# Kernel tuning notes

Measured on AMD Instinct MI355X. Metric: run time of the kernel, lower is better.

Reference implementation:

```python
import jax, jax.numpy as jnp
import numpy as np
from jax import lax

B, T, C = 4, 2048, 2048
HK, HV = 16, 16
DK, DV = 128, 128
KW = 4  # conv kernel width
KEY_DIM = HK * DK      # 2048
VAL_DIM = HV * DV      # 2048
QKV_DIM = 2 * KEY_DIM + VAL_DIM  # 6144
EPS_RMS = 1e-6
EPS_NORM = 1e-12


def setup_inputs() -> dict:
    key = jax.random.key(0)
    ks = jax.random.split(key, 7)
    s = 0.02
    x = jax.random.normal(ks[0], (B, T, C), dtype=jnp.float32)
    positions = jnp.broadcast_to(jnp.arange(T, dtype=jnp.int64 if jax.config.jax_enable_x64 else jnp.int32), (B, T))
    W_qkvz = jax.random.normal(ks[1], (C, QKV_DIM + VAL_DIM), dtype=jnp.float32) * s
    W_b = jax.random.normal(ks[2], (C, HV), dtype=jnp.float32) * s
    W_a = jax.random.normal(ks[3], (C, HV), dtype=jnp.float32) * s
    conv_w = jax.random.normal(ks[4], (QKV_DIM, 1, KW), dtype=jnp.float32) * 0.1
    norm_w = jnp.ones((DV,), dtype=jnp.float32)
    W_out = jax.random.normal(ks[5], (VAL_DIM, C), dtype=jnp.float32) * s
    return {"x": x, "positions": positions, "W_qkvz": W_qkvz, "W_b": W_b,
            "W_a": W_a, "conv_w": conv_w, "norm_w": norm_w, "W_out": W_out}


def _l2norm(u):
    n = jnp.sqrt(jnp.sum(u * u, axis=-1, keepdims=True))
    return u / jnp.maximum(n, EPS_NORM)


def _forward(x, W_qkvz, W_b, W_a, conv_w, norm_w, W_out):
    qkvz = x @ W_qkvz                               # [B,T,QKV+VAL]
    qkv, z = qkvz[..., :QKV_DIM], qkvz[..., QKV_DIM:]
    z = z.reshape(B, T, HV, DV)
    beta = jax.nn.sigmoid(x @ W_b)                  # [B,T,HV]
    alpha = jax.nn.sigmoid(x @ W_a)                 # [B,T,HV]

    # depthwise causal conv1d (padding K-1 then truncate to T)
    xc = jnp.transpose(qkv, (0, 2, 1))              # [B,QKV_DIM,T]
    xc = lax.conv_general_dilated(xc, conv_w, window_strides=(1,),
                                  padding=[(KW - 1, 0)],
                                  feature_group_count=QKV_DIM,
                                  dimension_numbers=("NCH", "OIH", "NCH"))
    qkv = jnp.transpose(jax.nn.silu(xc), (0, 2, 1))  # [B,T,QKV_DIM]

    q = _l2norm(qkv[..., :KEY_DIM].reshape(B, T, HK, DK))
    k = _l2norm(qkv[..., KEY_DIM:2 * KEY_DIM].reshape(B, T, HK, DK))
    v = qkv[..., 2 * KEY_DIM:].reshape(B, T, HV, DV)

    def step(state, inp):
        q_t, k_t, v_t, b_t, a_t = inp               # [B,H,DK],[B,H,DK],[B,H,DV],[B,H],[B,H]
        state = a_t[:, :, None, None] * state + \
                b_t[:, :, None, None] * (k_t[..., :, None] * v_t[:, :, None, :])
        out = jnp.einsum('bhk,bhkv->bhv', q_t, state)
        return state, out

    state0 = jnp.zeros((B, HK, DK, DV), dtype=x.dtype)
    seq = (jnp.moveaxis(q, 1, 0), jnp.moveaxis(k, 1, 0), jnp.moveaxis(v, 1, 0),
           jnp.moveaxis(beta, 1, 0), jnp.moveaxis(alpha, 1, 0))
    _, outs = lax.scan(step, state0, seq)           # [T,B,H,DV]
    out = jnp.moveaxis(outs, 0, 1)                  # [B,T,H,DV]

    # RMSNorm over head_v_dim (fp32), gated by sigmoid(z)
    of = out.astype(jnp.float32)
    rms = jnp.mean(of * of, axis=-1, keepdims=True)
    out = ((of * lax.rsqrt(rms + EPS_RMS)) * norm_w).astype(out.dtype)
    out = out * jax.nn.sigmoid(z)
    return out.reshape(B, T, VAL_DIM) @ W_out


def reference(x, positions, W_qkvz, W_b, W_a, conv_w, norm_w, W_out):
    return _forward(x, W_qkvz, W_b, W_a, conv_w, norm_w, W_out)
```

## Files before the change

kernel.cpp:

```cpp
#include <hip/hip_runtime.h>
#include <hip/hip_bf16.h>

typedef __bf16 bf16_t;
typedef __attribute__((ext_vector_type(8))) __bf16 bf16x8;
typedef __attribute__((ext_vector_type(4))) float floatx4;
typedef __attribute__((ext_vector_type(16))) float floatx16;


__device__ __forceinline__ void gload16(const void* g, void* l) {
  __builtin_amdgcn_global_load_lds(
      (const __attribute__((address_space(1))) void*)g,
      (__attribute__((address_space(3))) void*)l, 16, 0, 0);
}

__global__ __launch_bounds__(256) void k_cast_bf16(const float* __restrict__ in,
                                                   bf16_t* __restrict__ out) {
  long i = ((long)blockIdx.x * 256 + threadIdx.x) * 8;
  const float4 a = *(const float4*)(in + i);
  const float4 b = *(const float4*)(in + i + 4);
  bf16x8 o;
  o[0] = (bf16_t)a.x; o[1] = (bf16_t)a.y; o[2] = (bf16_t)a.z; o[3] = (bf16_t)a.w;
  o[4] = (bf16_t)b.x; o[5] = (bf16_t)b.y; o[6] = (bf16_t)b.z; o[7] = (bf16_t)b.w;
  *(bf16x8*)(out + i) = o;
}

__global__ void k_transpose_cast(const float* __restrict__ in, bf16_t* __restrict__ out,
                                 int R, int Ccols) {
  __shared__ float tile[32][33];
  int c0 = blockIdx.x * 32, r0 = blockIdx.y * 32;
  for (int i = threadIdx.y; i < 32; i += 8)
    tile[i][threadIdx.x] = in[(long)(r0 + i) * Ccols + c0 + threadIdx.x];
  __syncthreads();
  for (int i = threadIdx.y; i < 32; i += 8)
    out[(long)(c0 + i) * R + r0 + threadIdx.x] = (bf16_t)tile[threadIdx.x][i];
}

__global__ void k_transpose_f32(const float* __restrict__ in, float* __restrict__ out,
                                int R, int Ccols) {
  int r = blockIdx.x * blockDim.x + threadIdx.x;
  if (r < R)
    for (int c = 0; c < Ccols; ++c) out[(long)c * R + r] = in[(long)r * Ccols + c];
}

__global__ __launch_bounds__(256) void k_beta_alpha(const float* __restrict__ x,
                                                    const float* __restrict__ WbT,
                                                    const float* __restrict__ WaT,
                                                    float* __restrict__ beta,
                                                    float* __restrict__ alpha) {
  extern __shared__ float xs[];
  const long row0 = (long)blockIdx.x * 16;
  const int tid = threadIdx.x;
  {
    const float4* src = (const float4*)(x + row0 * 2048);
    float4* dst = (float4*)xs;
    for (int i = tid; i < 16 * 512; i += 256) dst[i] = src[i];
  }
  __syncthreads();
  const int wv = tid >> 6, lane = tid & 63;
  for (int oo = 0; oo < 8; ++oo) {
    const int o = wv * 8 + oo;
    const float* Wrow = (o < 16) ? (WbT + (long)o * 2048) : (WaT + (long)(o - 16) * 2048);
    float acc[16];
#pragma unroll
    for (int r = 0; r < 16; ++r) acc[r] = 0.f;
    for (int kc = 0; kc < 8; ++kc) {
      const float4 w4 = *(const float4*)(Wrow + kc * 256 + lane * 4);
#pragma unroll
      for (int r = 0; r < 16; ++r) {
        const float4 xv = *(const float4*)&xs[r * 2048 + kc * 256 + lane * 4];
        acc[r] += w4.x * xv.x + w4.y * xv.y + w4.z * xv.z + w4.w * xv.w;
      }
    }
#pragma unroll
    for (int r = 0; r < 16; ++r) {
      float s = acc[r];
      for (int off = 32; off; off >>= 1) s += __shfl_down(s, off);
      if (lane == 0) {
        const long row = row0 + r;
        const int b = (int)(row >> 11), t = (int)(row & 2047);
        const float sig = 1.f / (1.f + __expf(-s));
        float* dst = (o < 16) ? beta : alpha;
        dst[((long)(b * 16 + (o & 15))) * 2048 + t] = sig;
      }
    }
  }
}

template <typename OUT_T>
__global__ __launch_bounds__(512, 2) void k_gemm256(const bf16_t* __restrict__ A,
                                                    const bf16_t* __restrict__ Bt,
                                                    OUT_T* __restrict__ C,
                                                    int N, int K, int lda) {
  extern __shared__ char gsm[];
  const int m0 = blockIdx.y * 256, n0 = blockIdx.x * 256;
  const int tid = threadIdx.x;
  const int w = tid >> 6, l = tid & 63;
  const int wm = w >> 2, wn = w & 3;
  const int l31 = l & 31, l5 = l >> 5;

  const bf16_t* asrc[4];
  const bf16_t* bsrc[4];
  int dofs[4];
#pragma unroll
  for (int t = 0; t < 4; ++t) {
    int c = t * 512 + tid;
    int row = c >> 3, cs = (c & 7) ^ (row & 7);
    asrc[t] = A + (long)(m0 + row) * lda + cs * 8;
    bsrc[t] = Bt + (long)(n0 + row) * K + cs * 8;
    dofs[t] = c * 16;
  }

  auto STAGE = [&](int buf, int k0) {
    char* ab = gsm + buf * 65536;
    char* bb = ab + 32768;
#pragma unroll
    for (int t = 0; t < 4; ++t) {
      gload16(asrc[t] + k0, ab + dofs[t]);
      gload16(bsrc[t] + k0, bb + dofs[t]);
    }
  };

  floatx16 acc[4][2] = {};
  STAGE(0, 0);
  const int NK = K >> 6;
  for (int kt = 0; kt < NK; ++kt) {
    __syncthreads();
    if (kt + 1 < NK) STAGE((kt + 1) & 1, (kt + 1) << 6);
    const char* As_ = gsm + (kt & 1) * 65536;
    const char* Bs_ = As_ + 32768;
#pragma unroll
    for (int ks = 0; ks < 4; ++ks) {
      bf16x8 af[4], bfr[2];
#pragma unroll
      for (int mi = 0; mi < 4; ++mi) {
        const int r = wm * 128 + mi * 32 + l31;
        af[mi] = *(const bf16x8*)(As_ + r * 128 + (((ks * 2 + l5) ^ (r & 7)) << 4));
      }
#pragma unroll
      for (int ni = 0; ni < 2; ++ni) {
        const int r = wn * 64 + ni * 32 + l31;
        bfr[ni] = *(const bf16x8*)(Bs_ + r * 128 + (((ks * 2 + l5) ^ (r & 7)) << 4));
      }
      __builtin_amdgcn_s_setprio(1);
#pragma unroll
      for (int mi = 0; mi < 4; ++mi)
#pragma unroll
        for (int ni = 0; ni < 2; ++ni)
          acc[mi][ni] = __builtin_amdgcn_mfma_f32_32x32x16_bf16(af[mi], bfr[ni], acc[mi][ni], 0, 0, 0);
      __builtin_amdgcn_s_setprio(0);
    }
  }
  const int crow0 = m0 + wm * 128 + 4 * l5;
  const int ccol = n0 + wn * 64 + l31;
#pragma unroll
  for (int mi = 0; mi < 4; ++mi)
#pragma unroll
    for (int ni = 0; ni < 2; ++ni)
#pragma unroll
      for (int reg = 0; reg < 16; ++reg) {
        const int row = crow0 + mi * 32 + (reg & 3) + 8 * (reg >> 2);
        C[(long)row * N + ccol + ni * 32] = (OUT_T)acc[mi][ni][reg];
      }
}

__global__ __launch_bounds__(256) void k_conv(const bf16_t* __restrict__ qkvz,
                                              const float* __restrict__ conv_w,
                                              bf16_t* __restrict__ q, bf16_t* __restrict__ k,
                                              bf16_t* __restrict__ v) {
  int row = blockIdx.x;
  int b = row >> 11, t = row & 2047;
  __shared__ float ys[6144];
  __shared__ float gsum[32][9];
  __shared__ float norms[32];
  const int c0 = threadIdx.x * 8;
  for (int c8 = c0; c8 < 6144; c8 += 2048) {
    bf16x8 xr[4];
#pragma unroll
    for (int w2 = 0; w2 < 4; ++w2) {
      int tt = t - 3 + w2;
      bf16x8 zr = {};
      xr[w2] = (tt >= 0) ? *(const bf16x8*)&qkvz[((long)(b * 2048 + tt)) * 8192 + c8] : zr;
    }
#pragma unroll
    for (int j = 0; j < 8; ++j) {
      float4 wv = *(const float4*)&conv_w[(c8 + j) * 4];
      float a = (float)xr[0][j] * wv.x + (float)xr[1][j] * wv.y +
                (float)xr[2][j] * wv.z + (float)xr[3][j] * wv.w;
      ys[c8 + j] = a / (1.f + __expf(-a));
    }
  }
  __syncthreads();
  {
    int g = threadIdx.x >> 3, j = threadIdx.x & 7;
    float s = 0.f;
#pragma unroll
    for (int e = 0; e < 16; ++e) {
      float yv = ys[g * 128 + j * 16 + e];
      s += yv * yv;
    }
    gsum[g][j] = s;
  }
  __syncthreads();
  if (threadIdx.x < 32) {
    float s = 0.f;
#pragma unroll
    for (int j = 0; j < 8; j++) s += gsum[threadIdx.x][j];
    norms[threadIdx.x] = 1.f / fmaxf(sqrtf(s), 1e-12f);
  }
  __syncthreads();
  for (int c8 = c0; c8 < 6144; c8 += 2048) {
    float scale;
    bf16_t* dst;
    if (c8 < 2048) {
      int h = c8 >> 7;
      scale = norms[h];
      dst = q + (((long)(b * 16 + h)) * 2048 + t) * 128 + (c8 & 127);
    } else if (c8 < 4096) {
      int h = (c8 - 2048) >> 7;
      scale = norms[16 + h];
      dst = k + (((long)(b * 16 + h)) * 2048 + t) * 128 + (c8 & 127);
    } else {
      scale = 1.f;
      int h = (c8 - 4096) >> 7;
      dst = v + (((long)(b * 16 + h)) * 2048 + t) * 128 + (c8 & 127);
    }
    bf16x8 o;
#pragma unroll
    for (int j = 0; j < 8; ++j) o[j] = (bf16_t)(ys[c8 + j] * scale);
    *(bf16x8*)dst = o;
  }
}

__global__ __launch_bounds__(256) void k_tr_kv(const bf16_t* __restrict__ kv,
                                               const bf16_t* __restrict__ vv,
                                               bf16_t* __restrict__ qkvz) {
  __shared__ bf16_t t_lds[64 * 136];
  int bh = blockIdx.x >> 5, tc = blockIdx.x & 31;
  int t0 = tc * 64;
  int tid = threadIdx.x;
#pragma unroll
  for (int pass = 0; pass < 2; ++pass) {
    const bf16_t* src = (pass == 0 ? kv : vv) + (long)bh * 2048 * 128 + (long)t0 * 128;
    int r = tid >> 2, sc = (tid & 3) * 32;
    bf16x8 x0 = *(const bf16x8*)(src + (long)r * 128 + sc);
    bf16x8 x1 = *(const bf16x8*)(src + (long)r * 128 + sc + 8);
    bf16x8 x2 = *(const bf16x8*)(src + (long)r * 128 + sc + 16);
    bf16x8 x3 = *(const bf16x8*)(src + (long)r * 128 + sc + 24);
    __syncthreads();
    *(bf16x8*)&t_lds[r * 136 + sc] = x0;
    *(bf16x8*)&t_lds[r * 136 + sc + 8] = x1;
    *(bf16x8*)&t_lds[r * 136 + sc + 16] = x2;
    *(bf16x8*)&t_lds[r * 136 + sc + 24] = x3;
    __syncthreads();
    int d = tid >> 1, h2 = tid & 1;
    bf16_t* dst = qkvz + (long)(bh * 128 + d) * 8192 + (pass ? 4096 : 2048) + t0 + h2 * 32;
#pragma unroll
    for (int g = 0; g < 4; ++g) {
      bf16x8 o;
#pragma unroll
      for (int j = 0; j < 8; ++j) o[j] = t_lds[(h2 * 32 + g * 8 + j) * 136 + d];
      *(bf16x8*)(dst + g * 8) = o;
    }
  }
}

__global__ __launch_bounds__(512, 1) void k_scan_chunked(
    const bf16_t* __restrict__ qv, const bf16_t* __restrict__ kv,
    bf16_t* __restrict__ qkvz, float* __restrict__ so_hi,
    const float* __restrict__ beta, const float* __restrict__ alpha) {
  extern __shared__ char smem[];
  bf16_t* q_lds = (bf16_t*)smem;
  bf16_t* kn_lds = q_lds + 8704;
  bf16_t* kT_lds = kn_lds + 8704;
  bf16_t* vT_lds = kT_lds + 9216;
  bf16_t* P_lds = vT_lds + 2304;
  bf16_t* St_lds = P_lds + 4608;
  float* G_lds = (float*)(St_lds + 4352);
  float* bet_lds = G_lds + 64;
  float* w_lds = bet_lds + 64;
  float* eG_lds = w_lds + 64;

  const int bh = blockIdx.x, dvb = blockIdx.y;
  const int b = bh >> 4, h = bh & 15;
  const int tid = threadIdx.x;
  const int w = tid >> 6, l = tid & 63;
  const int l15 = l & 15, lg = l >> 4;
  const int g = w & 1, r = w >> 1;

  const bf16_t* qb = qv + (long)bh * 2048 * 128;
  const bf16_t* kb = kv + (long)bh * 2048 * 128;
  const bf16_t* kTg = qkvz + (long)bh * 128 * 8192 + 2048;
  const bf16_t* vTg = qkvz + (long)(bh * 128 + dvb * 32) * 8192 + 4096;
  const float* bet = beta + (long)bh * 2048;
  const float* alp = alpha + (long)bh * 2048;

  floatx4 streg[2] = {};
  for (int i = tid; i < 2176; i += 512) ((float*)St_lds)[i] = 0.f;
  __syncthreads();

  const int sr = tid >> 3, ssc = (tid & 7) * 16;
  const int sdk = tid >> 2, ssc2 = (tid & 3) * 16;

  for (int c = 0; c < 32; ++c) {
    const int t0 = c * 64;
    {
      const bf16_t* qs = qb + (long)(t0 + sr) * 128 + ssc;
      const bf16_t* ks = kb + (long)(t0 + sr) * 128 + ssc;
      const bf16_t* kts = kTg + (long)sdk * 8192 + t0 + ssc2;
      bf16x8 a0 = *(const bf16x8*)qs, a1 = *(const bf16x8*)(qs + 8);
      bf16x8 b0 = *(const bf16x8*)ks, b1 = *(const bf16x8*)(ks + 8);
      bf16x8 c0 = *(const bf16x8*)kts, c1 = *(const bf16x8*)(kts + 8);
      *(bf16x8*)&q_lds[sr * 136 + ssc] = a0;
      *(bf16x8*)&q_lds[sr * 136 + ssc + 8] = a1;
      *(bf16x8*)&kn_lds[sr * 136 + ssc] = b0;
      *(bf16x8*)&kn_lds[sr * 136 + ssc + 8] = b1;
      *(bf16x8*)&kT_lds[sdk * 72 + ssc2] = c0;
      *(bf16x8*)&kT_lds[sdk * 72 + ssc2 + 8] = c1;
      if (tid < 256) {
        int svr = tid >> 3, svc = (tid & 7) * 8;
        bf16x8 d0 = *(const bf16x8*)(vTg + (long)svr * 8192 + t0 + svc);
        *(bf16x8*)&vT_lds[svr * 72 + svc] = d0;
      }
      if (w == 0) {
        float bsv = bet[t0 + l];
        float la = __logf(alp[t0 + l]);
#pragma unroll
        for (int off = 1; off < 64; off <<= 1) {
          float xup = __shfl_up(la, off);
          if (l >= off) la += xup;
        }
        float ge = __shfl(la, 63);
        G_lds[l] = la;
        bet_lds[l] = bsv;
        w_lds[l] = bsv * __expf(ge - la);
        eG_lds[l] = __expf(la);
      }
    }
    __syncthreads();

    {
      bf16_t* p = &kT_lds[sdk * 72 + ssc2];
      bf16x8 x0 = *(bf16x8*)p, x1 = *(bf16x8*)(p + 8);
#pragma unroll
      for (int j = 0; j < 8; j++) {
        x0[j] = (bf16_t)((float)x0[j] * w_lds[ssc2 + j]);
        x1[j] = (bf16_t)((float)x1[j] * w_lds[ssc2 + 8 + j]);
      }
      *(bf16x8*)p = x0;
      *(bf16x8*)(p + 8) = x1;
    }

    {
      const int mi = w >> 1;
      bf16x8 aq[4];
#pragma unroll
      for (int ks = 0; ks < 4; ks++)
        aq[ks] = *(bf16x8*)&q_lds[(mi * 16 + l15) * 136 + ks * 32 + lg * 8];
#pragma unroll
      for (int sn2 = 0; sn2 < 2; sn2++) {
        const int sn = (w & 1) * 2 + sn2;
        floatx4 sc_ = {0.f, 0.f, 0.f, 0.f};
#pragma unroll
        for (int ks = 0; ks < 4; ks++) {
          bf16x8 bk = *(bf16x8*)&kn_lds[(sn * 16 + l15) * 136 + ks * 32 + lg * 8];
          sc_ = __builtin_amdgcn_mfma_f32_16x16x32_bf16(aq[ks], bk, sc_, 0, 0, 0);
        }
        const int sl = sn * 16 + l15;
        const float gs = G_lds[sl], bs = bet_lds[sl];
#pragma unroll
        for (int rr = 0; rr < 4; rr++) {
          const int tl = mi * 16 + lg * 4 + rr;
          float val = (sl <= tl) ? sc_[rr] * __expf(G_lds[tl] - gs) * bs : 0.f;
          P_lds[tl * 72 + sl] = (bf16_t)val;
        }
      }
    }
    __syncthreads();

    floatx4 acco = {0.f, 0.f, 0.f, 0.f};
    {
      const int rloc = g * 16 + l15;
      bf16x8 av0 = *(bf16x8*)&vT_lds[rloc * 72 + lg * 8];
      bf16x8 av1 = *(bf16x8*)&vT_lds[rloc * 72 + 32 + lg * 8];
      floatx4 f = {0.f, 0.f, 0.f, 0.f};
#pragma unroll
      for (int ks = 0; ks < 4; ks++) {
        bf16x8 aq = *(bf16x8*)&q_lds[(r * 16 + l15) * 136 + ks * 32 + lg * 8];
        bf16x8 bs_ = *(bf16x8*)&St_lds[rloc * 136 + ks * 32 + lg * 8];
        f = __builtin_amdgcn_mfma_f32_16x16x32_bf16(aq, bs_, f, 0, 0, 0);
      }
#pragma unroll
      for (int rr = 0; rr < 4; rr++) f[rr] *= eG_lds[r * 16 + lg * 4 + rr];
#pragma unroll
      for (int ks2 = 0; ks2 < 2; ks2++) {
        bf16x8 ap = *(bf16x8*)&P_lds[(r * 16 + l15) * 72 + ks2 * 32 + lg * 8];
        f = __builtin_amdgcn_mfma_f32_16x16x32_bf16(ap, (ks2 == 0) ? av0 : av1, f, 0, 0, 0);
      }
      acco = f;
      const float dcv = eG_lds[63];
#pragma unroll
      for (int ni = 0; ni < 2; ni++) {
        const int ni2 = r * 2 + ni;
#pragma unroll
        for (int rr = 0; rr < 4; rr++) streg[ni][rr] *= dcv;
        bf16x8 bk0 = *(bf16x8*)&kT_lds[(ni2 * 16 + l15) * 72 + lg * 8];
        bf16x8 bk1 = *(bf16x8*)&kT_lds[(ni2 * 16 + l15) * 72 + 32 + lg * 8];
        streg[ni] = __builtin_amdgcn_mfma_f32_16x16x32_bf16(av0, bk0, streg[ni], 0, 0, 0);
        streg[ni] = __builtin_amdgcn_mfma_f32_16x16x32_bf16(av1, bk1, streg[ni], 0, 0, 0);
      }
    }
    __syncthreads();

#pragma unroll
    for (int ni = 0; ni < 2; ni++) {
      const int ni2 = r * 2 + ni;
#pragma unroll
      for (int rr = 0; rr < 4; rr++)
        St_lds[(g * 16 + lg * 4 + rr) * 136 + ni2 * 16 + l15] = (bf16_t)streg[ni][rr];
    }
    {
      const int dvg = dvb * 32 + g * 16 + l15;
      const int hcol = h * 128 + dvg;
#pragma unroll
      for (int rr = 0; rr < 4; rr++) {
        const int t = t0 + r * 16 + lg * 4 + rr;
        const long row = (long)b * 2048 + t;
        if (hcol < 1024)
          ((float*)qkvz)[row * 4096 + hcol] = acco[rr];
        else
          so_hi[row * 1024 + hcol - 1024] = acco[rr];
      }
    }
  }
}

__global__ __launch_bounds__(256) void k_rmsgate(const float* __restrict__ so_hi,
                                                 const bf16_t* __restrict__ qkvz,
                                                 bf16_t* __restrict__ A2,
                                                 const float* __restrict__ norm_w) {
  long row = blockIdx.x;
  int tid = threadIdx.x;
  int h = tid >> 4, j = tid & 15;
  const float* srow = (h < 8) ? (const float*)qkvz + row * 4096 + h * 128 + j * 8
                              : so_hi + row * 1024 + (h - 8) * 128 + j * 8;
  float xv[8];
  *(float4*)&xv[0] = *(const float4*)srow;
  *(float4*)&xv[4] = *(const float4*)(srow + 4);
  float ss = 0.f;
#pragma unroll
  for (int e = 0; e < 8; e++) ss += xv[e] * xv[e];
  ss += __shfl_xor(ss, 1); ss += __shfl_xor(ss, 2);
  ss += __shfl_xor(ss, 4); ss += __shfl_xor(ss, 8);
  float rinv = rsqrtf(ss * (1.0f / 128.0f) + 1e-6f);
  const bf16_t* zrow = qkvz + row * 8192 + 6144 + h * 128 + j * 8;
  bf16x8 zv = *(const bf16x8*)zrow;
  bf16x8 o;
#pragma unroll
  for (int e = 0; e < 8; e++) {
    float z = (float)zv[e];
    float gate = 1.f / (1.f + __expf(-z));
    o[e] = (bf16_t)(xv[e] * rinv * norm_w[j * 8 + e] * gate);
  }
  *(bf16x8*)(A2 + row * 2048 + h * 128 + j * 8) = o;
}

extern "C" void kernel_launch(void* const* d_in, const int* in_sizes, int n_in,
                              void* d_out, int out_size, void* d_ws, size_t ws_size,
                              hipStream_t stream) {
  const float* x      = (const float*)d_in[0];
  const float* W_qkvz = (const float*)d_in[2];
  const float* W_b    = (const float*)d_in[3];
  const float* W_a    = (const float*)d_in[4];
  const float* conv_w = (const float*)d_in[5];
  const float* norm_w = (const float*)d_in[6];
  const float* W_out  = (const float*)d_in[7];
  float* out = (float*)d_out;
  char* ws = (char*)d_ws;

  bf16_t* qkvz  = (bf16_t*)(ws + 0);
  bf16_t* xb    = (bf16_t*)(ws + 134217728);
  bf16_t* qv    = (bf16_t*)(ws + 134217728);
  bf16_t* A2    = (bf16_t*)(ws + 134217728);
  bf16_t* WqT   = (bf16_t*)(ws + 167772160);
  bf16_t* kv    = (bf16_t*)(ws + 167772160);
  bf16_t* vv    = (bf16_t*)(ws + 201326592);
  float*  so_hi = (float*)(ws + 201326592);
  bf16_t* WoT   = (bf16_t*)(ws + 234881024);
  float*  WbT   = (float*)(ws + 243269632);
  float*  WaT   = (float*)(ws + 243400704);
  float*  beta  = (float*)(ws + 243531776);
  float*  alpha = (float*)(ws + 244056064);

  if (ws_size < 244580352) return;

  k_cast_bf16<<<8192, 256, 0, stream>>>(x, xb);
  k_transpose_cast<<<dim3(8192 / 32, 2048 / 32), dim3(32, 8), 0, stream>>>(W_qkvz, WqT, 2048, 8192);
  k_transpose_cast<<<dim3(2048 / 32, 2048 / 32), dim3(32, 8), 0, stream>>>(W_out, WoT, 2048, 2048);
  k_transpose_f32<<<8, 256, 0, stream>>>(W_b, WbT, 2048, 16);
  k_transpose_f32<<<8, 256, 0, stream>>>(W_a, WaT, 2048, 16);
  k_beta_alpha<<<512, 256, 131072, stream>>>(x, WbT, WaT, beta, alpha);
  k_gemm256<bf16_t><<<dim3(32, 32), 512, 131072, stream>>>(xb, WqT, qkvz, 8192, 2048, 2048);
  k_conv<<<8192, 256, 0, stream>>>(qkvz, conv_w, qv, kv, vv);
  k_tr_kv<<<2048, 256, 0, stream>>>(kv, vv, qkvz);
  k_scan_chunked<<<dim3(64, 4), 512, 76800, stream>>>(qv, kv, qkvz, so_hi, beta, alpha);
  k_rmsgate<<<8192, 256, 0, stream>>>(so_hi, qkvz, A2, norm_w);
  k_gemm256<float><<<dim3(8, 32), 512, 131072, stream>>>(A2, WoT, out, 2048, 2048, 2048);
  (void)in_sizes; (void)n_in; (void)out_size;
}
```

Measured before the change: 873.7 us.

## Switch GEMM to 16x16x32 MFMA and prefetch next chunk in recurrence kernel

The 256x256 GEMM now uses 16x16x32 bf16 MFMA tiles (8x4 accumulators per wave) in place of 32x32x16, which changes the LDS read pattern and the output store layout. Separately, the chunked delta-rule kernel loads the next chunk's q, k, kT, vT, beta and alpha from global memory into registers right after the barrier, so those loads overlap the current chunk's compute instead of stalling at its start. The cost is higher register pressure from the prefetch buffers and the larger accumulator array, which could reduce occupancy.

```diff
diff --git a/kernel.cpp b/kernel.cpp
--- a/kernel.cpp
+++ b/kernel.cpp
@@ -4,7 +4,6 @@
 typedef __bf16 bf16_t;
 typedef __attribute__((ext_vector_type(8))) __bf16 bf16x8;
 typedef __attribute__((ext_vector_type(4))) float floatx4;
-typedef __attribute__((ext_vector_type(16))) float floatx16;
 
 
 __device__ __forceinline__ void gload16(const void* g, void* l) {
@@ -96,7 +95,7 @@
   const int tid = threadIdx.x;
   const int w = tid >> 6, l = tid & 63;
   const int wm = w >> 2, wn = w & 3;
-  const int l31 = l & 31, l5 = l >> 5;
+  const int l15 = l & 15, lg = l >> 4;
 
   const bf16_t* asrc[4];
   const bf16_t* bsrc[4];
@@ -120,7 +119,7 @@
     }
   };
 
-  floatx16 acc[4][2] = {};
+  floatx4 acc[8][4] = {};
   STAGE(0, 0);
   const int NK = K >> 6;
   for (int kt = 0; kt < NK; ++kt) {
@@ -129,38 +128,36 @@
     const char* As_ = gsm + (kt & 1) * 65536;
     const char* Bs_ = As_ + 32768;
 #pragma unroll
-    for (int ks = 0; ks < 4; ++ks) {
-      bf16x8 af[4], bfr[2];
-#pragma unroll
-      for (int mi = 0; mi < 4; ++mi) {
-        const int r = wm * 128 + mi * 32 + l31;
-        af[mi] = *(const bf16x8*)(As_ + r * 128 + (((ks * 2 + l5) ^ (r & 7)) << 4));
-      }
-#pragma unroll
-      for (int ni = 0; ni < 2; ++ni) {
-        const int r = wn * 64 + ni * 32 + l31;
-        bfr[ni] = *(const bf16x8*)(Bs_ + r * 128 + (((ks * 2 + l5) ^ (r & 7)) << 4));
+    for (int ks = 0; ks < 2; ++ks) {
+      bf16x8 af[8], bfr[4];
+#pragma unroll
+      for (int mi = 0; mi < 8; ++mi) {
+        const int r = wm * 128 + mi * 16 + l15;
+        af[mi] = *(const bf16x8*)(As_ + r * 128 + ((((ks << 2) + lg) ^ (r & 7)) << 4));
+      }
+#pragma unroll
+      for (int ni = 0; ni < 4; ++ni) {
+        const int r = wn * 64 + ni * 16 + l15;
+        bfr[ni] = *(const bf16x8*)(Bs_ + r * 128 + ((((ks << 2) + lg) ^ (r & 7)) << 4));
       }
       __builtin_amdgcn_s_setprio(1);
 #pragma unroll
-      for (int mi = 0; mi < 4; ++mi)
-#pragma unroll
-        for (int ni = 0; ni < 2; ++ni)
-          acc[mi][ni] = __builtin_amdgcn_mfma_f32_32x32x16_bf16(af[mi], bfr[ni], acc[mi][ni], 0, 0, 0);
+      for (int mi = 0; mi < 8; ++mi)
+#pragma unroll
+        for (int ni = 0; ni < 4; ++ni)
+          acc[mi][ni] = __builtin_amdgcn_mfma_f32_16x16x32_bf16(af[mi], bfr[ni], acc[mi][ni], 0, 0, 0);
       __builtin_amdgcn_s_setprio(0);
     }
   }
-  const int crow0 = m0 + wm * 128 + 4 * l5;
-  const int ccol = n0 + wn * 64 + l31;
-#pragma unroll
-  for (int mi = 0; mi < 4; ++mi)
-#pragma unroll
-    for (int ni = 0; ni < 2; ++ni)
-#pragma unroll
-      for (int reg = 0; reg < 16; ++reg) {
-        const int row = crow0 + mi * 32 + (reg & 3) + 8 * (reg >> 2);
-        C[(long)row * N + ccol + ni * 32] = (OUT_T)acc[mi][ni][reg];
-      }
+  const int crow0 = m0 + wm * 128 + lg * 4;
+  const int ccol = n0 + wn * 64 + l15;
+#pragma unroll
+  for (int mi = 0; mi < 8; ++mi)
+#pragma unroll
+    for (int ni = 0; ni < 4; ++ni)
+#pragma unroll
+      for (int r = 0; r < 4; ++r)
+        C[(long)(crow0 + mi * 16 + r) * N + ccol + ni * 16] = (OUT_T)acc[mi][ni][r];
 }
 
 __global__ __launch_bounds__(256) void k_conv(const bf16_t* __restrict__ qkvz,
@@ -300,30 +297,34 @@
 
   const int sr = tid >> 3, ssc = (tid & 7) * 16;
   const int sdk = tid >> 2, ssc2 = (tid & 3) * 16;
+  const int svr = tid >> 3, svc = (tid & 7) * 8;
+
+  bf16x8 ra0, ra1, rb0, rb1, rc0, rc1, rd0 = {};
+  float rbet = 0.f, ralp = 1.f;
+  {
+    const bf16_t* qs = qb + (long)sr * 128 + ssc;
+    const bf16_t* ks = kb + (long)sr * 128 + ssc;
+    const bf16_t* kts = kTg + (long)sdk * 8192 + ssc2;
+    ra0 = *(const bf16x8*)qs; ra1 = *(const bf16x8*)(qs + 8);
+    rb0 = *(const bf16x8*)ks; rb1 = *(const bf16x8*)(ks + 8);
+    rc0 = *(const bf16x8*)kts; rc1 = *(const bf16x8*)(kts + 8);
+    if (tid < 256) rd0 = *(const bf16x8*)(vTg + (long)svr * 8192 + svc);
+    if (w == 0) { rbet = bet[l]; ralp = alp[l]; }
+  }
 
   for (int c = 0; c < 32; ++c) {
     const int t0 = c * 64;
     {
-      const bf16_t* qs = qb + (long)(t0 + sr) * 128 + ssc;
-      const bf16_t* ks = kb + (long)(t0 + sr) * 128 + ssc;
-      const bf16_t* kts = kTg + (long)sdk * 8192 + t0 + ssc2;
-      bf16x8 a0 = *(const bf16x8*)qs, a1 = *(const bf16x8*)(qs + 8);
-      bf16x8 b0 = *(const bf16x8*)ks, b1 = *(const bf16x8*)(ks + 8);
-      bf16x8 c0 = *(const bf16x8*)kts, c1 = *(const bf16x8*)(kts + 8);
-      *(bf16x8*)&q_lds[sr * 136 + ssc] = a0;
-      *(bf16x8*)&q_lds[sr * 136 + ssc + 8] = a1;
-      *(bf16x8*)&kn_lds[sr * 136 + ssc] = b0;
-      *(bf16x8*)&kn_lds[sr * 136 + ssc + 8] = b1;
-      *(bf16x8*)&kT_lds[sdk * 72 + ssc2] = c0;
-      *(bf16x8*)&kT_lds[sdk * 72 + ssc2 + 8] = c1;
-      if (tid < 256) {
-        int svr = tid >> 3, svc = (tid & 7) * 8;
-        bf16x8 d0 = *(const bf16x8*)(vTg + (long)svr * 8192 + t0 + svc);
-        *(bf16x8*)&vT_lds[svr * 72 + svc] = d0;
-      }
+      *(bf16x8*)&q_lds[sr * 136 + ssc] = ra0;
+      *(bf16x8*)&q_lds[sr * 136 + ssc + 8] = ra1;
+      *(bf16x8*)&kn_lds[sr * 136 + ssc] = rb0;
+      *(bf16x8*)&kn_lds[sr * 136 + ssc + 8] = rb1;
+      *(bf16x8*)&kT_lds[sdk * 72 + ssc2] = rc0;
+      *(bf16x8*)&kT_lds[sdk * 72 + ssc2 + 8] = rc1;
+      if (tid < 256) *(bf16x8*)&vT_lds[svr * 72 + svc] = rd0;
       if (w == 0) {
-        float bsv = bet[t0 + l];
-        float la = __logf(alp[t0 + l]);
+        float bsv = rbet;
+        float la = __logf(ralp);
 #pragma unroll
         for (int off = 1; off < 64; off <<= 1) {
           float xup = __shfl_up(la, off);
@@ -337,6 +338,18 @@
       }
     }
     __syncthreads();
+
+    if (c + 1 < 32) {
+      const int t1 = t0 + 64;
+      const bf16_t* qs = qb + (long)(t1 + sr) * 128 + ssc;
+      const bf16_t* ks = kb + (long)(t1 + sr) * 128 + ssc;
+      const bf16_t* kts = kTg + (long)sdk * 8192 + t1 + ssc2;
+      ra0 = *(const bf16x8*)qs; ra1 = *(const bf16x8*)(qs + 8);
+      rb0 = *(const bf16x8*)ks; rb1 = *(const bf16x8*)(ks + 8);
+      rc0 = *(const bf16x8*)kts; rc1 = *(const bf16x8*)(kts + 8);
+      if (tid < 256) rd0 = *(const bf16x8*)(vTg + (long)svr * 8192 + t1 + svc);
+      if (w == 0) { rbet = bet[t1 + l]; ralp = alp[t1 + l]; }
+    }
 
     {
       bf16_t* p = &kT_lds[sdk * 72 + ssc2];
```

New measurement: 821.8 us. 1.06x faster.
